# Performance work log

Hardware: AMD Instinct MI355X
Metric: run time of the kernel (lower is better)

The kernel has to match this reference:

```python
import jax, jax.numpy as jnp
import numpy as np

INV_SQRT2 = 0.7071067811865476


def _quadrature_ops(d):
    # truncated harmonic-oscillator ladder operator: a[n, n+1] = sqrt(n+1)
    a = jnp.diag(jnp.sqrt(jnp.arange(1, d, dtype=jnp.float32)), k=1)
    X0 = (a + a.T) * INV_SQRT2
    P0 = (a - a.T) * INV_SQRT2  # real-valued stand-in for the momentum quadrature
    I = jnp.eye(d, dtype=jnp.float32)
    return I, X0, P0


def setup_inputs() -> dict:
    key = jax.random.key(0)
    ks = jax.random.split(key, 6)
    D, d, w, K = 512, 32, 8, 4
    return {
        "mps_params": jax.random.normal(ks[0], (D, d, D), dtype=jnp.float32),
        "theta": jax.random.normal(ks[1], (1,), dtype=jnp.float32),
        "env_L": jax.random.normal(ks[2], (K, D, w, D), dtype=jnp.float32) * 0.1,
        "env_R": jax.random.normal(ks[3], (K, D, w, D), dtype=jnp.float32) * 0.1,
        "coeffs": jax.random.normal(ks[4], (K, w, w, 5), dtype=jnp.float32),
        "prefactors": jax.random.normal(ks[5], (K,), dtype=jnp.float32),
    }


def reference(mps_params, theta, env_L, env_R, coeffs, prefactors):
    A = mps_params  # [D(left), d(phys), D(right)]
    d = A.shape[1]
    K = prefactors.shape[0]

    # norm_fn: psi.H @ psi for a single-tensor MPS is sum(A^2)
    An = A / jnp.sqrt(jnp.sum(A * A))

    # _get_XandP: quadrature rotation from basis params
    I, X0, P0 = _quadrature_ops(d)
    c, s = jnp.cos(theta[0]), jnp.sin(theta[0])
    X = c * X0 + s * P0
    P = -s * X0 + c * P0

    # dynamic MPO cores: W_k[i,j] = sum_c coeffs[k,i,j,c] * ops[c]
    ops = jnp.stack([I, X, P, X @ X, P @ P])  # [5, d, d]
    W = jnp.einsum('kijc,cab->kijab', coeffs, ops)  # [K, w, w, d, d]

    out = jnp.zeros((), dtype=A.dtype)
    for k in range(K):  # fixed small loop over Hamiltonian constituents
        # T: [L, w, p, r]
        T = jnp.einsum('Lwl,lpr->Lwpr', env_L[k], An)
        # apply MPO core: [L, v, P, r]
        T = jnp.einsum('wvPp,Lwpr->LvPr', W[k], T)
        # close with right env: [L, P, R]
        T = jnp.einsum('LvPr,Rvr->LPR', T, env_R[k])
        out = out + prefactors[k] * jnp.einsum('LPR,LPR->', An, T)
    return out
```

## Files before the change

### kernel.cpp

```cpp
#include <hip/hip_runtime.h>


typedef __attribute__((ext_vector_type(8))) _Float16 f16x8;
typedef __attribute__((ext_vector_type(4))) float f32x4;

#define RPS 280

__device__ __forceinline__ unsigned short f2h(float f) {
    _Float16 h = (_Float16)f;
    return *(unsigned short*)&h;
}

__device__ __forceinline__ void gload16(const void* g, void* l) {
    __builtin_amdgcn_global_load_lds(
        (const __attribute__((address_space(1))) void*)g,
        (__attribute__((address_space(3))) void*)l, 16, 0, 0);
}

struct GArg {
    const unsigned short* A;
    const unsigned short* B;
    unsigned short* C;
    int kshift;
    long long kextra;
};

__device__ __forceinline__ void stage_tile(
    const GArg& g, int srow0, int col0, int kt0,
    short* dstA, short* dstB, int tid)
{
    #pragma unroll
    for (int q = 0; q < 4; ++q) {
        const int c = q * 512 + tid;
        const int r = c >> 3;
        const int gs = (c & 7) ^ (r & 7);
        const int gr = srow0 + r;
        const size_t aoff = (size_t)gr * 512 + (size_t)((unsigned)gr >> g.kshift) * g.kextra;
        gload16(g.A + aoff + kt0 + gs * 8, dstA + c * 8);
        gload16(g.B + (size_t)(col0 + r) * 512 + kt0 + gs * 8, dstB + c * 8);
    }
}

__global__ __launch_bounds__(512, 1) void gemm_dual_mega(int K, int NPB, GArg g0, GArg g1)
{
    __shared__ short lds[74496];
    const GArg g = blockIdx.z ? g1 : g0;
    const int tid = threadIdx.x;
    const int wid = tid >> 6, lane = tid & 63;
    const int wm = wid >> 2, wn = wid & 3;
    const int lrow = lane & 15, lgrp = lane >> 4;
    const int sx = lrow & 7;
    const int gsw0 = (lgrp ^ sx) * 8, gsw1 = ((lgrp + 4) ^ sx) * 8;

    const int xcd = blockIdx.x & 7, loc = blockIdx.x >> 3;
    const int col0 = (xcd * 8 + loc) * 256;
    const int row_base = blockIdx.y * NPB * 256;

    short* A0 = lds;          short* B0 = lds + 16384;
    short* A1 = lds + 32768;  short* B1 = lds + 49152;
    short* repk = lds + 65536;

    const int NT = (K >> 6) * NPB;

    f32x4 acc[8][4] = {};

    stage_tile(g, row_base, col0, 0, A0, B0, tid);
    stage_tile(g, row_base, col0, 64, A1, B1, tid);
    asm volatile("s_waitcnt vmcnt(8)" ::: "memory");
    __builtin_amdgcn_s_barrier();
    __builtin_amdgcn_sched_barrier(0);

    for (int it = 0; it < NT; ++it) {
        const short* cA = (it & 1) ? A1 : A0;
        const short* cB = (it & 1) ? B1 : B0;
        short* wA = (it & 1) ? A1 : A0;
        short* wB = (it & 1) ? B1 : B0;

        f16x8 bfr[4][2], afr[4][2];
        #pragma unroll
        for (int j = 0; j < 4; ++j) {
            const int R = wn * 64 + j * 16 + lrow;
            bfr[j][0] = *(const f16x8*)&cB[R * 64 + gsw0];
            bfr[j][1] = *(const f16x8*)&cB[R * 64 + gsw1];
        }
        #pragma unroll
        for (int i = 0; i < 4; ++i) {
            const int R = wm * 128 + i * 16 + lrow;
            afr[i][0] = *(const f16x8*)&cA[R * 64 + gsw0];
            afr[i][1] = *(const f16x8*)&cA[R * 64 + gsw1];
        }
        __builtin_amdgcn_s_setprio(1);
        #pragma unroll
        for (int i = 0; i < 4; ++i)
            #pragma unroll
            for (int j = 0; j < 4; ++j) {
                acc[i][j] = __builtin_amdgcn_mfma_f32_16x16x32_f16(afr[i][0], bfr[j][0], acc[i][j], 0, 0, 0);
                acc[i][j] = __builtin_amdgcn_mfma_f32_16x16x32_f16(afr[i][1], bfr[j][1], acc[i][j], 0, 0, 0);
            }
        __builtin_amdgcn_s_setprio(0);
        #pragma unroll
        for (int i = 0; i < 4; ++i) {
            const int R = wm * 128 + (i + 4) * 16 + lrow;
            afr[i][0] = *(const f16x8*)&cA[R * 64 + gsw0];
            afr[i][1] = *(const f16x8*)&cA[R * 64 + gsw1];
        }
        asm volatile("s_waitcnt lgkmcnt(0)" ::: "memory");
        __builtin_amdgcn_sched_barrier(0);
        __builtin_amdgcn_s_barrier();
        __builtin_amdgcn_sched_barrier(0);
        if (it + 2 < NT) {
            const int it2 = it + 2;
            stage_tile(g, row_base + (it2 >> 3) * 256, col0, (it2 & 7) * 64, wA, wB, tid);
        }
        __builtin_amdgcn_s_setprio(1);
        #pragma unroll
        for (int i = 0; i < 4; ++i)
            #pragma unroll
            for (int j = 0; j < 4; ++j) {
                acc[i + 4][j] = __builtin_amdgcn_mfma_f32_16x16x32_f16(afr[i][0], bfr[j][0], acc[i + 4][j], 0, 0, 0);
                acc[i + 4][j] = __builtin_amdgcn_mfma_f32_16x16x32_f16(afr[i][1], bfr[j][1], acc[i + 4][j], 0, 0, 0);
            }
        __builtin_amdgcn_s_setprio(0);
        __builtin_amdgcn_sched_barrier(0);
        if (it + 2 < NT) asm volatile("s_waitcnt vmcnt(8)" ::: "memory");
        else             asm volatile("s_waitcnt vmcnt(0)" ::: "memory");
        __builtin_amdgcn_sched_barrier(0);
        __builtin_amdgcn_s_barrier();
        __builtin_amdgcn_sched_barrier(0);

        if ((it & 7) == 7) {
            const int row0 = row_base + (it >> 3) * 256;
            const int orow = lgrp * 4, ocol = lrow;
            #pragma unroll
            for (int c8 = 0; c8 < 8; ++c8) {
                if (wm == (c8 >> 2)) {
                    const int ib = (c8 & 3) * 2;
                    #pragma unroll
                    for (int di = 0; di < 2; ++di)
                        #pragma unroll
                        for (int j = 0; j < 4; ++j)
                            #pragma unroll
                            for (int q = 0; q < 4; ++q)
                                repk[(di * 16 + orow + q) * RPS + wn * 64 + j * 16 + ocol] =
                                    (short)f2h(acc[ib + di][j][q]);
                }
                asm volatile("s_waitcnt lgkmcnt(0)" ::: "memory");
                __builtin_amdgcn_s_barrier();
                #pragma unroll
                for (int s2 = 0; s2 < 2; ++s2) {
                    const int idx = s2 * 512 + tid;
                    const int rr = idx >> 5, cc = idx & 31;
                    *(int4*)(g.C + (size_t)(row0 + c8 * 32 + rr) * 16384 + col0 + cc * 8) =
                        *(const int4*)&repk[rr * RPS + cc * 8];
                }
                asm volatile("s_waitcnt lgkmcnt(0)" ::: "memory");
                __builtin_amdgcn_s_barrier();
            }
            #pragma unroll
            for (int i = 0; i < 8; ++i)
                #pragma unroll
                for (int j = 0; j < 4; ++j)
                    acc[i][j] = (f32x4){0.f, 0.f, 0.f, 0.f};
        }
    }
}

__global__ __launch_bounds__(1024) void gemm_g4w(
    const unsigned short* __restrict__ T1, const unsigned short* __restrict__ Yp,
    const float* __restrict__ W2p, float* __restrict__ dacc,
    int Lt8, int zkShift, int BKC)
{
    __shared__ short sh[16384];
    const int tid = threadIdx.x;
    const int wid = tid >> 6, lane = tid & 63;
    const int kidx = blockIdx.x >> zkShift;
    const int kz = (blockIdx.x - (kidx << zkShift)) * BKC;
    const int wr = (wid >> 2) * 64, wc = (wid & 3) * 64;
    const int lrow = lane & 15, kb = (lane >> 4) * 8;

    const int r = tid >> 2, kc = (tid & 3) * 8;
    const int w_ = r >> 5, p_ = r & 31;
    const size_t T1k = (size_t)kidx * Lt8 * 16384;
    const size_t Yk = (size_t)kidx * 4096;
    const size_t aoff = T1k + (size_t)w_ * 16384 + (size_t)p_ * 512;
    const size_t boff = Yk + (size_t)p_ * 16384 + (size_t)w_ * 512;

    f32x4 acc[4][4] = {};

    for (int k0 = 0; k0 < BKC; k0 += 32) {
        const int kk = kz + k0;
        const int lt = kk >> 9, rbase = kk & 511;
        gload16(T1 + aoff + (size_t)lt * 131072 + rbase + kc, sh + tid * 8);
        gload16(Yp + boff + (size_t)lt * 524288 + rbase + kc, sh + 8192 + tid * 8);
        __syncthreads();
        f16x8 a[4], b[4];
        #pragma unroll
        for (int i = 0; i < 4; ++i)
            a[i] = *(const f16x8*)&sh[(wr + i * 16 + lrow) * 32 + kb];
        #pragma unroll
        for (int j = 0; j < 4; ++j)
            b[j] = *(const f16x8*)&sh[8192 + (wc + j * 16 + lrow) * 32 + kb];
        #pragma unroll
        for (int i = 0; i < 4; ++i)
            #pragma unroll
            for (int j = 0; j < 4; ++j)
                acc[i][j] = __builtin_amdgcn_mfma_f32_16x16x32_f16(a[i], b[j], acc[i][j], 0, 0, 0);
        __syncthreads();
    }

    const int orow = (lane >> 4) * 4, ocol = lane & 15;
    const float* Wk = W2p + ((size_t)kidx << 16);
    float s = 0.f;
    #pragma unroll
    for (int j = 0; j < 4; ++j) {
        const int n = wc + j * 16 + ocol;
        const float* wrow = Wk + (size_t)n * 256 + wr + orow;
        #pragma unroll
        for (int i = 0; i < 4; ++i) {
            float4 wv = *(const float4*)(wrow + i * 16);
            s += wv.x * acc[i][j][0] + wv.y * acc[i][j][1]
               + wv.z * acc[i][j][2] + wv.w * acc[i][j][3];
        }
    }
    __syncthreads();
    float* red = (float*)sh;
    red[tid] = s;
    __syncthreads();
    for (int st = 512; st > 0; st >>= 1) {
        if (tid < st) red[tid] += red[tid + st];
        __syncthreads();
    }
    if (tid == 0) atomicAdd(dacc, red[0]);
}

__global__ __launch_bounds__(256) void cast_sumsq(
    const float* __restrict__ in, unsigned short* __restrict__ out,
    long long n4, float* __restrict__ sumsq)
{
    float p = 0.f;
    for (long long i = (long long)blockIdx.x * blockDim.x + threadIdx.x; i < n4;
         i += (long long)gridDim.x * blockDim.x) {
        float4 v = ((const float4*)in)[i];
        p += v.x * v.x + v.y * v.y + v.z * v.z + v.w * v.w;
        union { unsigned short s[4]; uint2 d; } o;
        o.s[0] = f2h(v.x); o.s[1] = f2h(v.y); o.s[2] = f2h(v.z); o.s[3] = f2h(v.w);
        ((uint2*)out)[i] = o.d;
    }
    __shared__ float sh[256];
    sh[threadIdx.x] = p;
    __syncthreads();
    for (int s = 128; s > 0; s >>= 1) {
        if (threadIdx.x < s) sh[threadIdx.x] += sh[threadIdx.x + s];
        __syncthreads();
    }
    if (threadIdx.x == 0) atomicAdd(sumsq, sh[0]);
}

__global__ void cast_kernel(const float* __restrict__ in, unsigned short* __restrict__ out,
                            long long n4)
{
    for (long long i = (long long)blockIdx.x * blockDim.x + threadIdx.x; i < n4;
         i += (long long)gridDim.x * blockDim.x) {
        float4 v = ((const float4*)in)[i];
        union { unsigned short s[4]; uint2 d; } o;
        o.s[0] = f2h(v.x); o.s[1] = f2h(v.y); o.s[2] = f2h(v.z); o.s[3] = f2h(v.w);
        ((uint2*)out)[i] = o.d;
    }
}

__global__ void transpose_cast(const float* __restrict__ in, unsigned short* __restrict__ out,
                               int R, int C, long long in_stride, long long out_stride)
{
    __shared__ float tile[32][33];
    in += (long long)blockIdx.z * in_stride;
    out += (long long)blockIdx.z * out_stride;
    int c0 = blockIdx.x * 32, r0 = blockIdx.y * 32;
    int tx = threadIdx.x, ty = threadIdx.y;
    #pragma unroll
    for (int i = 0; i < 4; ++i)
        tile[ty + i * 8][tx] = in[(size_t)(r0 + ty + i * 8) * C + c0 + tx];
    __syncthreads();
    #pragma unroll
    for (int i = 0; i < 4; ++i)
        out[(size_t)(c0 + ty + i * 8) * R + r0 + tx] = f2h(tile[tx][ty + i * 8]);
}

__global__ void build_ops(const float* __restrict__ theta, float* __restrict__ ops)
{
    __shared__ float X[32][32], Pm[32][32];
    int i = threadIdx.y, j = threadIdx.x;
    float c = cosf(theta[0]), s = sinf(theta[0]);
    float aij = (j == i + 1) ? sqrtf((float)j) : 0.f;
    float aji = (i == j + 1) ? sqrtf((float)i) : 0.f;
    const float inv = 0.70710678118654752440f;
    float x0 = (aij + aji) * inv;
    float p0 = (aij - aji) * inv;
    X[i][j] = c * x0 + s * p0;
    Pm[i][j] = -s * x0 + c * p0;
    __syncthreads();
    float xx = 0.f, pp = 0.f;
    #pragma unroll
    for (int m = 0; m < 32; ++m) {
        xx += X[i][m] * X[m][j];
        pp += Pm[i][m] * Pm[m][j];
    }
    ops[0 * 1024 + i * 32 + j] = (i == j) ? 1.f : 0.f;
    ops[1 * 1024 + i * 32 + j] = X[i][j];
    ops[2 * 1024 + i * 32 + j] = Pm[i][j];
    ops[3 * 1024 + i * 32 + j] = xx;
    ops[4 * 1024 + i * 32 + j] = pp;
}

__global__ void build_w(const float* __restrict__ coeffs, const float* __restrict__ ops,
                        const float* __restrict__ pref, float* __restrict__ W2)
{
    int b = blockIdx.x;
    int k = b >> 6, w = (b >> 3) & 7, v = b & 7;
    int P = threadIdx.y, p = threadIdx.x;
    const float* cf = coeffs + ((k * 8 + w) * 8 + v) * 5;
    float acc = 0.f;
    #pragma unroll
    for (int c = 0; c < 5; ++c) acc += cf[c] * ops[c * 1024 + P * 32 + p];
    W2[(size_t)k * 65536 + (v * 32 + P) * 256 + (w * 32 + p)] = acc * pref[k];
}

__global__ void finalize_kernel(const float* __restrict__ dacc, const float* __restrict__ sumsq,
                                float* __restrict__ out)
{
    if (threadIdx.x == 0) out[0] = dacc[0] / sumsq[0];
}

extern "C" void kernel_launch(void* const* d_in, const int* in_sizes, int n_in,
                              void* d_out, int out_size, void* d_ws, size_t ws_size,
                              hipStream_t stream)
{
    const float* A      = (const float*)d_in[0];
    const float* theta  = (const float*)d_in[1];
    const float* envL   = (const float*)d_in[2];
    const float* envR   = (const float*)d_in[3];
    const float* coeffs = (const float*)d_in[4];
    const float* pref   = (const float*)d_in[5];
    float* out = (float*)d_out;

    char* ws = (char*)d_ws;
    float* sumsq = (float*)ws;
    float* dacc  = (float*)(ws + 4);
    float* ops   = (float*)(ws + 64);
    float* W2    = (float*)(ws + (32 << 10));
    unsigned short* envLh  = (unsigned short*)(ws + (4ull << 20));
    unsigned short* Ah     = (unsigned short*)(ws + (21ull << 20));
    unsigned short* Ath    = (unsigned short*)(ws + (38ull << 20));
    unsigned short* envRth = (unsigned short*)(ws + (55ull << 20));
    const size_t big0 = 72ull << 20;

    int Lt = 512;
    while (Lt > 16) {
        size_t need = big0 + 2ull * (size_t)Lt * (1ull << 20);
        if (need <= ws_size) break;
        Lt >>= 1;
    }
    unsigned short* T1 = (unsigned short*)(ws + big0);
    unsigned short* Yp = T1 + (size_t)Lt * 524288;

    const int Lt8 = Lt * 8;
    const int kshiftA = __builtin_ctz(Lt8);
    const long long kextraA = 2097152LL - (long long)Lt8 * 512;
    const int NPB = (Lt >= 16) ? (Lt / 16) : 1;
    const int KT = Lt * 512;
    const int BKC = 256;
    const int zk = KT / BKC;
    const int zkShift = __builtin_ctz(zk);

    hipMemsetAsync(ws, 0, 64, stream);

    cast_sumsq<<<1024, 256, 0, stream>>>(A, Ah, 2097152LL, sumsq);
    build_ops<<<1, dim3(32, 32), 0, stream>>>(theta, ops);
    build_w<<<256, dim3(32, 32), 0, stream>>>(coeffs, ops, pref, W2);
    cast_kernel<<<2048, 256, 0, stream>>>(envL, envLh, 2097152LL);
    transpose_cast<<<dim3(512, 16, 1), dim3(32, 8), 0, stream>>>(A, Ath, 512, 16384, 0, 0);
    transpose_cast<<<dim3(128, 16, 4), dim3(32, 8), 0, stream>>>(envR, envRth, 512, 4096,
                                                                 2097152LL, 2097152LL);

    const int ntiles = 512 / Lt;
    for (int t = 0; t < ntiles; ++t) {
        GArg g0, g1;
        g0.A = envLh + (size_t)t * Lt8 * 512; g0.B = Ath; g0.C = T1;
        g0.kshift = kshiftA; g0.kextra = kextraA;
        g1.A = Ah + (size_t)t * Lt * 16384; g1.B = envRth; g1.C = Yp;
        g1.kshift = 30; g1.kextra = 0;
        gemm_dual_mega<<<dim3(64, 2, 2), 512, 0, stream>>>(512, NPB, g0, g1);
        gemm_g4w<<<dim3(4 * zk), 1024, 0, stream>>>(T1, Yp, W2, dacc, Lt8, zkShift, BKC);
    }
    finalize_kernel<<<1, 64, 0, stream>>>(dacc, sumsq, out);
}
```

Baseline: 1.126 ms.

## Shrink GEMM tiles to 256x128xK32 for multiple blocks per CU

The dual GEMM kernel moves from 256x256 tiles with K-step 64 and one block per CU to 256x128 tiles with K-step 32, using a smaller LDS footprint, half the accumulators, and launch bounds allowing four blocks per CU. The grid doubles in the column dimension and the LDS swizzle, staging and epilogue are adapted to the narrower tile. Separately, the K-chunk size for the second GEMM now scales with the tile size instead of being fixed. Higher occupancy is meant to hide latency and fill more CUs, at the cost of more barriers per unit of work and lower data reuse per block.

```diff
diff --git a/kernel.cpp b/kernel.cpp
--- a/kernel.cpp
+++ b/kernel.cpp
@@ -3,8 +3,6 @@
 
 typedef __attribute__((ext_vector_type(8))) _Float16 f16x8;
 typedef __attribute__((ext_vector_type(4))) float f32x4;
-
-#define RPS 280
 
 __device__ __forceinline__ unsigned short f2h(float f) {
     _Float16 h = (_Float16)f;
@@ -25,48 +23,54 @@
     long long kextra;
 };
 
-__device__ __forceinline__ void stage_tile(
+__device__ __forceinline__ void stage32(
     const GArg& g, int srow0, int col0, int kt0,
     short* dstA, short* dstB, int tid)
 {
     #pragma unroll
-    for (int q = 0; q < 4; ++q) {
+    for (int q = 0; q < 2; ++q) {
         const int c = q * 512 + tid;
-        const int r = c >> 3;
-        const int gs = (c & 7) ^ (r & 7);
-        const int gr = srow0 + r;
+        const int row = c >> 2;
+        const int gs = (c & 3) ^ (row & 3);
+        const int gr = srow0 + row;
         const size_t aoff = (size_t)gr * 512 + (size_t)((unsigned)gr >> g.kshift) * g.kextra;
         gload16(g.A + aoff + kt0 + gs * 8, dstA + c * 8);
-        gload16(g.B + (size_t)(col0 + r) * 512 + kt0 + gs * 8, dstB + c * 8);
-    }
-}
-
-__global__ __launch_bounds__(512, 1) void gemm_dual_mega(int K, int NPB, GArg g0, GArg g1)
-{
-    __shared__ short lds[74496];
+    }
+    {
+        const int c = tid;
+        const int row = c >> 2;
+        const int gs = (c & 3) ^ (row & 3);
+        gload16(g.B + (size_t)(col0 + row) * 512 + kt0 + gs * 8, dstB + c * 8);
+    }
+}
+
+__global__ __launch_bounds__(512, 4) void gemm_dual_mega(int NPB, GArg g0, GArg g1)
+{
+    __shared__ short lds[28928];
     const GArg g = blockIdx.z ? g1 : g0;
     const int tid = threadIdx.x;
     const int wid = tid >> 6, lane = tid & 63;
-    const int wm = wid >> 2, wn = wid & 3;
+    const int wm = wid >> 1, wn = wid & 1;
     const int lrow = lane & 15, lgrp = lane >> 4;
-    const int sx = lrow & 7;
-    const int gsw0 = (lgrp ^ sx) * 8, gsw1 = ((lgrp + 4) ^ sx) * 8;
+    const int rdoff = lrow * 32 + ((lgrp ^ (lrow & 3)) * 8);
 
     const int xcd = blockIdx.x & 7, loc = blockIdx.x >> 3;
-    const int col0 = (xcd * 8 + loc) * 256;
+    const int col0 = (xcd * 16 + loc) * 128;
     const int row_base = blockIdx.y * NPB * 256;
 
-    short* A0 = lds;          short* B0 = lds + 16384;
-    short* A1 = lds + 32768;  short* B1 = lds + 49152;
-    short* repk = lds + 65536;
-
-    const int NT = (K >> 6) * NPB;
-
-    f32x4 acc[8][4] = {};
-
-    stage_tile(g, row_base, col0, 0, A0, B0, tid);
-    stage_tile(g, row_base, col0, 64, A1, B1, tid);
-    asm volatile("s_waitcnt vmcnt(8)" ::: "memory");
+    short* A0 = lds;
+    short* A1 = lds + 8192;
+    short* B0 = lds + 16384;
+    short* B1 = lds + 20480;
+    short* repk = lds + 24576;
+
+    const int NT = NPB * 16;
+
+    f32x4 acc[4][4] = {};
+
+    stage32(g, row_base, col0, 0, A0, B0, tid);
+    stage32(g, row_base, col0, 32, A1, B1, tid);
+    asm volatile("s_waitcnt vmcnt(3)" ::: "memory");
     __builtin_amdgcn_s_barrier();
     __builtin_amdgcn_sched_barrier(0);
 
@@ -76,88 +80,63 @@
         short* wA = (it & 1) ? A1 : A0;
         short* wB = (it & 1) ? B1 : B0;
 
-        f16x8 bfr[4][2], afr[4][2];
-        #pragma unroll
-        for (int j = 0; j < 4; ++j) {
-            const int R = wn * 64 + j * 16 + lrow;
-            bfr[j][0] = *(const f16x8*)&cB[R * 64 + gsw0];
-            bfr[j][1] = *(const f16x8*)&cB[R * 64 + gsw1];
-        }
-        #pragma unroll
-        for (int i = 0; i < 4; ++i) {
-            const int R = wm * 128 + i * 16 + lrow;
-            afr[i][0] = *(const f16x8*)&cA[R * 64 + gsw0];
-            afr[i][1] = *(const f16x8*)&cA[R * 64 + gsw1];
+        f16x8 afr[4], bfr[4];
+        #pragma unroll
+        for (int j = 0; j < 4; ++j)
+            bfr[j] = *(const f16x8*)&cB[(wn * 64 + j * 16) * 32 + rdoff];
+        #pragma unroll
+        for (int i = 0; i < 4; ++i)
+            afr[i] = *(const f16x8*)&cA[(wm * 64 + i * 16) * 32 + rdoff];
+        asm volatile("s_waitcnt lgkmcnt(0)" ::: "memory");
+        __builtin_amdgcn_sched_barrier(0);
+        __builtin_amdgcn_s_barrier();
+        __builtin_amdgcn_sched_barrier(0);
+        if (it + 2 < NT) {
+            const int it2 = it + 2;
+            stage32(g, row_base + (it2 >> 4) * 256, col0, (it2 & 15) * 32, wA, wB, tid);
         }
         __builtin_amdgcn_s_setprio(1);
         #pragma unroll
         for (int i = 0; i < 4; ++i)
             #pragma unroll
-            for (int j = 0; j < 4; ++j) {
-                acc[i][j] = __builtin_amdgcn_mfma_f32_16x16x32_f16(afr[i][0], bfr[j][0], acc[i][j], 0, 0, 0);
-                acc[i][j] = __builtin_amdgcn_mfma_f32_16x16x32_f16(afr[i][1], bfr[j][1], acc[i][j], 0, 0, 0);
-            }
+            for (int j = 0; j < 4; ++j)
+                acc[i][j] = __builtin_amdgcn_mfma_f32_16x16x32_f16(afr[i], bfr[j], acc[i][j], 0, 0, 0);
         __builtin_amdgcn_s_setprio(0);
-        #pragma unroll
-        for (int i = 0; i < 4; ++i) {
-            const int R = wm * 128 + (i + 4) * 16 + lrow;
-            afr[i][0] = *(const f16x8*)&cA[R * 64 + gsw0];
-            afr[i][1] = *(const f16x8*)&cA[R * 64 + gsw1];
-        }
-        asm volatile("s_waitcnt lgkmcnt(0)" ::: "memory");
+        __builtin_amdgcn_sched_barrier(0);
+        if (it + 2 < NT) asm volatile("s_waitcnt vmcnt(3)" ::: "memory");
+        else             asm volatile("s_waitcnt vmcnt(0)" ::: "memory");
         __builtin_amdgcn_sched_barrier(0);
         __builtin_amdgcn_s_barrier();
         __builtin_amdgcn_sched_barrier(0);
-        if (it + 2 < NT) {
-            const int it2 = it + 2;
-            stage_tile(g, row_base + (it2 >> 3) * 256, col0, (it2 & 7) * 64, wA, wB, tid);
-        }
-        __builtin_amdgcn_s_setprio(1);
-        #pragma unroll
-        for (int i = 0; i < 4; ++i)
-            #pragma unroll
-            for (int j = 0; j < 4; ++j) {
-                acc[i + 4][j] = __builtin_amdgcn_mfma_f32_16x16x32_f16(afr[i][0], bfr[j][0], acc[i + 4][j], 0, 0, 0);
-                acc[i + 4][j] = __builtin_amdgcn_mfma_f32_16x16x32_f16(afr[i][1], bfr[j][1], acc[i + 4][j], 0, 0, 0);
-            }
-        __builtin_amdgcn_s_setprio(0);
-        __builtin_amdgcn_sched_barrier(0);
-        if (it + 2 < NT) asm volatile("s_waitcnt vmcnt(8)" ::: "memory");
-        else             asm volatile("s_waitcnt vmcnt(0)" ::: "memory");
-        __builtin_amdgcn_sched_barrier(0);
-        __builtin_amdgcn_s_barrier();
-        __builtin_amdgcn_sched_barrier(0);
-
-        if ((it & 7) == 7) {
-            const int row0 = row_base + (it >> 3) * 256;
+
+        if ((it & 15) == 15) {
+            const int row0 = row_base + (it >> 4) * 256;
             const int orow = lgrp * 4, ocol = lrow;
             #pragma unroll
             for (int c8 = 0; c8 < 8; ++c8) {
-                if (wm == (c8 >> 2)) {
-                    const int ib = (c8 & 3) * 2;
+                if (wm == (c8 >> 1)) {
+                    const int ib = (c8 & 1) * 2;
                     #pragma unroll
                     for (int di = 0; di < 2; ++di)
                         #pragma unroll
                         for (int j = 0; j < 4; ++j)
                             #pragma unroll
                             for (int q = 0; q < 4; ++q)
-                                repk[(di * 16 + orow + q) * RPS + wn * 64 + j * 16 + ocol] =
+                                repk[(di * 16 + orow + q) * 136 + wn * 64 + j * 16 + ocol] =
                                     (short)f2h(acc[ib + di][j][q]);
                 }
                 asm volatile("s_waitcnt lgkmcnt(0)" ::: "memory");
                 __builtin_amdgcn_s_barrier();
-                #pragma unroll
-                for (int s2 = 0; s2 < 2; ++s2) {
-                    const int idx = s2 * 512 + tid;
-                    const int rr = idx >> 5, cc = idx & 31;
+                {
+                    const int rr = tid >> 4, cc = tid & 15;
                     *(int4*)(g.C + (size_t)(row0 + c8 * 32 + rr) * 16384 + col0 + cc * 8) =
-                        *(const int4*)&repk[rr * RPS + cc * 8];
+                        *(const int4*)&repk[rr * 136 + cc * 8];
                 }
                 asm volatile("s_waitcnt lgkmcnt(0)" ::: "memory");
                 __builtin_amdgcn_s_barrier();
             }
             #pragma unroll
-            for (int i = 0; i < 8; ++i)
+            for (int i = 0; i < 4; ++i)
                 #pragma unroll
                 for (int j = 0; j < 4; ++j)
                     acc[i][j] = (f32x4){0.f, 0.f, 0.f, 0.f};
@@ -365,9 +344,9 @@
     const int Lt8 = Lt * 8;
     const int kshiftA = __builtin_ctz(Lt8);
     const long long kextraA = 2097152LL - (long long)Lt8 * 512;
-    const int NPB = (Lt >= 16) ? (Lt / 16) : 1;
+    const int NPB = Lt / 16;
     const int KT = Lt * 512;
-    const int BKC = 256;
+    int BKC = KT / 64; if (BKC < 128) BKC = 128;
     const int zk = KT / BKC;
     const int zkShift = __builtin_ctz(zk);
 
@@ -388,7 +367,7 @@
         g0.kshift = kshiftA; g0.kextra = kextraA;
         g1.A = Ah + (size_t)t * Lt * 16384; g1.B = envRth; g1.C = Yp;
         g1.kshift = 30; g1.kextra = 0;
-        gemm_dual_mega<<<dim3(64, 2, 2), 512, 0, stream>>>(512, NPB, g0, g1);
+        gemm_dual_mega<<<dim3(128, 2, 2), 512, 0, stream>>>(NPB, g0, g1);
         gemm_g4w<<<dim3(4 * zk), 1024, 0, stream>>>(T1, Yp, W2, dacc, Lt8, zkShift, BKC);
     }
     finalize_kernel<<<1, 64, 0, stream>>>(dacc, sumsq, out);
```

Result: faster. 1.098 ms (-2.5%).

## Retile g4w GEMM to 512 threads with larger per-warp tiles and swizzled LDS

Applied to the files above, without the earlier changes.

The second GEMM kernel moves from 1024 to 512 threads per block, with each wave computing an 8x4 grid of MFMA tiles instead of 4x4. Each thread now issues two async global-to-LDS loads per k-step, and the LDS column layout is XOR-swizzled to reduce bank conflicts. The split-K chunk doubles, halving the number of blocks and atomic reductions. The dual mega GEMM also loosens its vmcnt wait at the row-tile boundary to keep more loads in flight. In exchange, register pressure per thread rises and fewer blocks are available to fill the device.

```diff
diff --git a/kernel.cpp b/kernel.cpp
--- a/kernel.cpp
+++ b/kernel.cpp
@@ -122,8 +122,14 @@
             }
         __builtin_amdgcn_s_setprio(0);
         __builtin_amdgcn_sched_barrier(0);
-        if (it + 2 < NT) asm volatile("s_waitcnt vmcnt(8)" ::: "memory");
-        else             asm volatile("s_waitcnt vmcnt(0)" ::: "memory");
+        if (it + 2 < NT) {
+            if ((it & 7) == 0 && it != 0)
+                asm volatile("s_waitcnt vmcnt(24)" ::: "memory");
+            else
+                asm volatile("s_waitcnt vmcnt(8)" ::: "memory");
+        } else {
+            asm volatile("s_waitcnt vmcnt(0)" ::: "memory");
+        }
         __builtin_amdgcn_sched_barrier(0);
         __builtin_amdgcn_s_barrier();
         __builtin_amdgcn_sched_barrier(0);
@@ -165,7 +171,7 @@
     }
 }
 
-__global__ __launch_bounds__(1024) void gemm_g4w(
+__global__ __launch_bounds__(512, 1) void gemm_g4w(
     const unsigned short* __restrict__ T1, const unsigned short* __restrict__ Yp,
     const float* __restrict__ W2p, float* __restrict__ dacc,
     int Lt8, int zkShift, int BKC)
@@ -175,48 +181,54 @@
     const int wid = tid >> 6, lane = tid & 63;
     const int kidx = blockIdx.x >> zkShift;
     const int kz = (blockIdx.x - (kidx << zkShift)) * BKC;
-    const int wr = (wid >> 2) * 64, wc = (wid & 3) * 64;
-    const int lrow = lane & 15, kb = (lane >> 4) * 8;
-
-    const int r = tid >> 2, kc = (tid & 3) * 8;
-    const int w_ = r >> 5, p_ = r & 31;
+    const int wm = wid >> 2, wn = wid & 3;
+    const int lrow = lane & 15, lgrp = lane >> 4;
+    const int rdoff = lrow * 32 + ((lgrp ^ ((lrow >> 1) & 3)) * 8);
+
     const size_t T1k = (size_t)kidx * Lt8 * 16384;
     const size_t Yk = (size_t)kidx * 4096;
-    const size_t aoff = T1k + (size_t)w_ * 16384 + (size_t)p_ * 512;
-    const size_t boff = Yk + (size_t)p_ * 16384 + (size_t)w_ * 512;
-
-    f32x4 acc[4][4] = {};
+
+    f32x4 acc[8][4] = {};
 
     for (int k0 = 0; k0 < BKC; k0 += 32) {
         const int kk = kz + k0;
         const int lt = kk >> 9, rbase = kk & 511;
-        gload16(T1 + aoff + (size_t)lt * 131072 + rbase + kc, sh + tid * 8);
-        gload16(Yp + boff + (size_t)lt * 524288 + rbase + kc, sh + 8192 + tid * 8);
+        #pragma unroll
+        for (int q = 0; q < 2; ++q) {
+            const int c = q * 512 + tid;
+            const int row = c >> 2;
+            const int gs = (c & 3) ^ ((row >> 1) & 3);
+            const int hi = row >> 5, lo = row & 31;
+            gload16(T1 + T1k + (size_t)(lt * 8 + hi) * 16384 + lo * 512 + rbase + gs * 8,
+                    sh + c * 8);
+            gload16(Yp + Yk + (size_t)(lt * 32 + lo) * 16384 + hi * 512 + rbase + gs * 8,
+                    sh + 8192 + c * 8);
+        }
         __syncthreads();
-        f16x8 a[4], b[4];
-        #pragma unroll
-        for (int i = 0; i < 4; ++i)
-            a[i] = *(const f16x8*)&sh[(wr + i * 16 + lrow) * 32 + kb];
+        f16x8 a[8], b[4];
         #pragma unroll
         for (int j = 0; j < 4; ++j)
-            b[j] = *(const f16x8*)&sh[8192 + (wc + j * 16 + lrow) * 32 + kb];
-        #pragma unroll
-        for (int i = 0; i < 4; ++i)
+            b[j] = *(const f16x8*)&sh[8192 + (wn * 64 + j * 16) * 32 + rdoff];
+        #pragma unroll
+        for (int i = 0; i < 8; ++i)
+            a[i] = *(const f16x8*)&sh[(wm * 128 + i * 16) * 32 + rdoff];
+        #pragma unroll
+        for (int i = 0; i < 8; ++i)
             #pragma unroll
             for (int j = 0; j < 4; ++j)
                 acc[i][j] = __builtin_amdgcn_mfma_f32_16x16x32_f16(a[i], b[j], acc[i][j], 0, 0, 0);
         __syncthreads();
     }
 
-    const int orow = (lane >> 4) * 4, ocol = lane & 15;
+    const int orow = lgrp * 4, ocol = lrow;
     const float* Wk = W2p + ((size_t)kidx << 16);
     float s = 0.f;
     #pragma unroll
     for (int j = 0; j < 4; ++j) {
-        const int n = wc + j * 16 + ocol;
-        const float* wrow = Wk + (size_t)n * 256 + wr + orow;
-        #pragma unroll
-        for (int i = 0; i < 4; ++i) {
+        const int n = wn * 64 + j * 16 + ocol;
+        const float* wrow = Wk + (size_t)n * 256 + wm * 128 + orow;
+        #pragma unroll
+        for (int i = 0; i < 8; ++i) {
             float4 wv = *(const float4*)(wrow + i * 16);
             s += wv.x * acc[i][j][0] + wv.y * acc[i][j][1]
                + wv.z * acc[i][j][2] + wv.w * acc[i][j][3];
@@ -226,7 +238,7 @@
     float* red = (float*)sh;
     red[tid] = s;
     __syncthreads();
-    for (int st = 512; st > 0; st >>= 1) {
+    for (int st = 256; st > 0; st >>= 1) {
         if (tid < st) red[tid] += red[tid + st];
         __syncthreads();
     }
@@ -365,9 +377,9 @@
     const int Lt8 = Lt * 8;
     const int kshiftA = __builtin_ctz(Lt8);
     const long long kextraA = 2097152LL - (long long)Lt8 * 512;
-    const int NPB = (Lt >= 16) ? (Lt / 16) : 1;
+    const int NPB = Lt / 16;
     const int KT = Lt * 512;
-    const int BKC = 256;
+    const int BKC = 512;
     const int zk = KT / BKC;
     const int zkShift = __builtin_ctz(zk);
 
@@ -389,7 +401,7 @@
         g1.A = Ah + (size_t)t * Lt * 16384; g1.B = envRth; g1.C = Yp;
         g1.kshift = 30; g1.kextra = 0;
         gemm_dual_mega<<<dim3(64, 2, 2), 512, 0, stream>>>(512, NPB, g0, g1);
-        gemm_g4w<<<dim3(4 * zk), 1024, 0, stream>>>(T1, Yp, W2, dacc, Lt8, zkShift, BKC);
+        gemm_g4w<<<dim3(4 * zk), 512, 0, stream>>>(T1, Yp, W2, dacc, Lt8, zkShift, BKC);
     }
     finalize_kernel<<<1, 64, 0, stream>>>(dacc, sumsq, out);
 }
```

Measured after the change: 1.027 ms. 1.1x faster.
